# Optimization experiments

Measured on AMD Instinct MI355X. Metric: run time of the kernel, lower is better.

The kernel has to match this reference:

```python
import jax, jax.numpy as jnp
import numpy as np

L, B, H, S, V, D = 2, 128, 1024, 512, 32000, 64
W_SCALE = 0.02

def setup_inputs() -> dict:
    key = jax.random.key(0)
    ks = jax.random.split(key, 17)
    f = lambda k, shape: jax.random.normal(k, shape, dtype=jnp.float32)
    return {
        "input_ids": jax.random.randint(ks[0], (1, B), 0, V),
        "h": f(ks[1], (L, B, H)),
        "c": f(ks[2], (L, B, H)),
        "h_s": f(ks[3], (S, B, H)),
        "emb": f(ks[4], (V, H)),
        "W_pt": f(ks[5], (H, H)) * W_SCALE,
        "b_pt": f(ks[6], (H,)) * W_SCALE,
        "v_pt": f(ks[7], (H,)) * W_SCALE,
        "b_v": f(ks[8], (1,)) * W_SCALE,
        "W_a": f(ks[9], (H, H)) * W_SCALE,
        "b_a": f(ks[10], (1,)) * W_SCALE,
        "W_ih": f(ks[11], (L, 4 * H, H)) * W_SCALE,
        "W_hh": f(ks[12], (L, 4 * H, H)) * W_SCALE,
        "b_ih": f(ks[13], (L, 4 * H)) * W_SCALE,
        "b_hh": f(ks[14], (L, 4 * H)) * W_SCALE,
        "W_out": f(ks[15], (V, H)) * W_SCALE,
        "b_out": f(ks[16], (V,)) * W_SCALE,
    }


def reference(input_ids, h, c, h_s, emb, W_pt, b_pt, v_pt, b_v, W_a, b_a,
              W_ih, W_hh, b_ih, b_hh, W_out, b_out):
    S_len = h_s.shape[0]
    x_emb = emb[input_ids]                     # [1, B, H]
    h_top = h[-1]                              # [B, H] top-layer decoder state
    # predicted alignment position p_t = S * sigmoid(v . tanh(W h + b))
    p_t = S_len * jax.nn.sigmoid(jnp.tanh(h_top @ W_pt.T + b_pt) @ v_pt + b_v[0])  # [B]
    s = jnp.clip(jnp.round(p_t).astype(jnp.int32), D, S_len - 1 - D)               # [B]
    # gather local window h_s[s-D : s+D+1] per batch element
    idx = s[:, None] + jnp.arange(-D, D + 1)    # [B, 2D+1]
    h_s_b = jnp.transpose(h_s, (1, 0, 2))       # [B, S, H]
    h_loc = jnp.take_along_axis(h_s_b, idx[:, :, None], axis=1)  # [B, 2D+1, H]
    # bilinear score h_t^T W_a h_s_j per window position
    scores = jnp.einsum('bh,hk,bjk->bj', h_top, W_a, h_loc) + b_a[0]  # [B, 2D+1]
    sigma2 = (D / 2.0) ** 2
    gauss = jnp.exp(-((idx.astype(p_t.dtype) - p_t[:, None]) ** 2) / (2.0 * sigma2))
    a_t = jax.nn.softmax(scores, axis=-1) * gauss                      # [B, 2D+1]
    context = jnp.einsum('bj,bjh->bh', a_t, h_loc)                     # [B, H]
    # inject context into the LSTM hidden state, then run one step
    h_in = h + context[None]                    # [L, B, H]
    x = x_emb[0]                                # [B, H]
    hs, cs = [], []
    for l in range(h.shape[0]):
        gates = x @ W_ih[l].T + b_ih[l] + h_in[l] @ W_hh[l].T + b_hh[l]
        i, f, g, o = jnp.split(gates, 4, axis=-1)
        c_new = jax.nn.sigmoid(f) * c[l] + jax.nn.sigmoid(i) * jnp.tanh(g)
        h_new = jax.nn.sigmoid(o) * jnp.tanh(c_new)
        hs.append(h_new)
        cs.append(c_new)
        x = h_new
    h_out = jnp.stack(hs)                       # [L, B, H]
    c_out = jnp.stack(cs)                       # [L, B, H]
    logits = jax.nn.log_softmax(x @ W_out.T + b_out, axis=-1)  # [B, V]
    return logits, h_out, c_out, context, s
```

## Files before the change

### kernel.cpp

```cpp
#include <hip/hip_runtime.h>
#include <hip/hip_bf16.h>
#include <math.h>

typedef __bf16 bf16_8 __attribute__((ext_vector_type(8)));
typedef __bf16 bf16_4 __attribute__((ext_vector_type(4)));
typedef float  f32x4  __attribute__((ext_vector_type(4)));

static __device__ __forceinline__ float sigmoidf_(float x){ return 1.0f/(1.0f + expf(-x)); }

#define BB 128
#define HH 1024
#define SS 512
#define VV 32000

#define OFF_A0    0u
#define OFF_A1    524288u
#define OFF_ALOG  1048576u
#define OFF_AH    1310720u
#define OFF_AM    1572864u
#define OFF_AL    1835008u
#define OFF_WAT   2097152u
#define OFF_Q     6291456u
#define OFF_Z     6815744u
#define OFF_PT    7340032u
#define OFF_SI    7340544u
#define OFF_SC    7341056u
#define OFF_G0P   7408640u
#define OFF_G1P   24185856u
#define OFF_PMAX  40963072u
#define OFF_PSUM  41225216u

__global__ void k_prep_all(const float* __restrict__ W_a, float* __restrict__ WaT,
                           const int* __restrict__ ids, const float* __restrict__ emb,
                           const float* __restrict__ h, const float* __restrict__ b_pt,
                           __bf16* __restrict__ A0, __bf16* __restrict__ Ah,
                           __bf16* __restrict__ Am, __bf16* __restrict__ Al,
                           float* __restrict__ z, float* __restrict__ q){
  __shared__ float tsm[32][33];
  int blk = blockIdx.x, t = threadIdx.x;
  if (blk < 1024){
    int kt = blk & 31, nt = blk >> 5;
    int c = t & 31, r0 = t >> 5;
    #pragma unroll
    for (int i = 0; i < 4; ++i){
      int r = r0 + 8*i;
      tsm[r][c] = W_a[(size_t)(kt*32 + r)*HH + nt*32 + c];
    }
    __syncthreads();
    #pragma unroll
    for (int i = 0; i < 4; ++i){
      int r = r0 + 8*i;
      WaT[(size_t)(nt*32 + r)*HH + kt*32 + c] = tsm[c][r];
    }
  } else {
    int b = blk - 1024, c = t*4;
    int tok = ids[b];
    f32x4 e = *(const f32x4*)(emb + (size_t)tok*HH + c);
    bf16_4 e4;
    #pragma unroll
    for (int i=0;i<4;i++) e4[i] = (__bf16)e[i];
    *(bf16_4*)(A0 + (size_t)b*2048 + c) = e4;
    f32x4 x = *(const f32x4*)(h + (size_t)BB*HH + (size_t)b*HH + c);
    bf16_4 hi4, mi4, lo4;
    #pragma unroll
    for (int i=0;i<4;i++){
      float v = x[i];
      __bf16 bh = (__bf16)v; float r1 = v - (float)bh;
      __bf16 bm = (__bf16)r1; float r2 = r1 - (float)bm;
      hi4[i]=bh; mi4[i]=bm; lo4[i]=(__bf16)r2;
    }
    *(bf16_4*)(Ah + (size_t)b*HH + c) = hi4;
    *(bf16_4*)(Am + (size_t)b*HH + c) = mi4;
    *(bf16_4*)(Al + (size_t)b*HH + c) = lo4;
    *(f32x4*)(z + (size_t)b*HH + c) = *(const f32x4*)(b_pt + c);
    *(f32x4*)(q + (size_t)b*HH + c) = f32x4{0.f,0.f,0.f,0.f};
  }
}

template<int PREC>
__device__ __forceinline__ void gemm_small(
    char* smem,
    const __bf16* __restrict__ Ah, const __bf16* __restrict__ Am, const __bf16* __restrict__ Al,
    int lda, const float* __restrict__ B1, int K,
    float* __restrict__ C, int N, int xblk, int ysplit)
{
  constexpr int NS   = PREC;
  constexpr int BK   = 32;
  constexpr int KG   = BK/8;
  constexpr int TILE = 128*BK*2;
  constexpr int UPT  = (128*KG)/256;
  char* sA = smem;
  char* sB = smem + NS*TILE;

  const int t = threadIdx.x;
  const int lane = t & 63, wave = t >> 6;
  const int wm = wave >> 1, wn = wave & 1;
  const int quad = lane >> 4, ln = lane & 15;
  const int nblock = xblk * 128;
  const int kchunk = K / ysplit;
  const int kstart = blockIdx.y * kchunk;
  const int kend = kstart + kchunk;

  f32x4 acc[4][4];
  #pragma unroll
  for (int i=0;i<4;i++)
    #pragma unroll
    for (int j=0;j<4;j++) acc[i][j] = f32x4{0.f,0.f,0.f,0.f};

  for (int k0 = kstart; k0 < kend; k0 += BK){
    #pragma unroll
    for (int i = 0; i < UPT; ++i){
      int u = t + 256*i;
      int row = u / KG, kg = u % KG;
      int sl = row*(BK*2) + (((kg ^ (row & (KG-1)))) << 4);
      *(uint4*)(sA + sl) = *(const uint4*)(Ah + (size_t)row*lda + k0 + kg*8);
      if constexpr (PREC >= 2)
        *(uint4*)(sA + TILE + sl) = *(const uint4*)(Am + (size_t)row*lda + k0 + kg*8);
      if constexpr (PREC >= 3)
        *(uint4*)(sA + 2*TILE + sl) = *(const uint4*)(Al + (size_t)row*lda + k0 + kg*8);
      int ng = nblock + row;
      const float* src = B1 + (size_t)ng*K + k0 + kg*8;
      f32x4 x0 = *(const f32x4*)(src);
      f32x4 x1 = *(const f32x4*)(src + 4);
      bf16_8 hi, mi, lo;
      #pragma unroll
      for (int qv=0;qv<8;qv++){
        float v = (qv<4) ? x0[qv] : x1[qv-4];
        __bf16 bh = (__bf16)v;
        hi[qv] = bh;
        float r1 = v - (float)bh;
        __bf16 bm = (__bf16)r1;
        mi[qv] = bm;
        lo[qv] = (__bf16)(r1 - (float)bm);
      }
      *(bf16_8*)(sB + sl) = hi;
      if constexpr (PREC >= 2) *(bf16_8*)(sB + TILE + sl) = mi;
      if constexpr (PREC >= 3) *(bf16_8*)(sB + 2*TILE + sl) = lo;
    }
    __syncthreads();
    {
      bf16_8 af[NS][4], bfr[NS][4];
      #pragma unroll
      for (int mt=0; mt<4; ++mt){
        int row = wm*64 + mt*16 + ln;
        int kg = quad;
        int sl = row*(BK*2) + (((kg ^ (row & (KG-1)))) << 4);
        #pragma unroll
        for (int s=0;s<NS;s++) af[s][mt] = *(const bf16_8*)(sA + s*TILE + sl);
      }
      #pragma unroll
      for (int nt=0; nt<4; ++nt){
        int row = wn*64 + nt*16 + ln;
        int kg = quad;
        int sl = row*(BK*2) + (((kg ^ (row & (KG-1)))) << 4);
        #pragma unroll
        for (int s=0;s<NS;s++) bfr[s][nt] = *(const bf16_8*)(sB + s*TILE + sl);
      }
      #pragma unroll
      for (int mt=0; mt<4; ++mt)
        #pragma unroll
        for (int nt=0; nt<4; ++nt){
          acc[mt][nt] = __builtin_amdgcn_mfma_f32_16x16x32_bf16(af[0][mt], bfr[0][nt], acc[mt][nt], 0,0,0);
          if constexpr (PREC >= 2){
            acc[mt][nt] = __builtin_amdgcn_mfma_f32_16x16x32_bf16(af[0][mt], bfr[1][nt], acc[mt][nt], 0,0,0);
            acc[mt][nt] = __builtin_amdgcn_mfma_f32_16x16x32_bf16(af[1][mt], bfr[0][nt], acc[mt][nt], 0,0,0);
          }
          if constexpr (PREC >= 3){
            acc[mt][nt] = __builtin_amdgcn_mfma_f32_16x16x32_bf16(af[0][mt], bfr[2][nt], acc[mt][nt], 0,0,0);
            acc[mt][nt] = __builtin_amdgcn_mfma_f32_16x16x32_bf16(af[1][mt], bfr[1][nt], acc[mt][nt], 0,0,0);
            acc[mt][nt] = __builtin_amdgcn_mfma_f32_16x16x32_bf16(af[2][mt], bfr[0][nt], acc[mt][nt], 0,0,0);
          }
        }
    }
    __syncthreads();
  }

  #pragma unroll
  for (int nt=0; nt<4; ++nt){
    int n = nblock + wn*64 + nt*16 + ln;
    #pragma unroll
    for (int mt=0; mt<4; ++mt){
      int m0 = wm*64 + mt*16 + quad*4;
      #pragma unroll
      for (int r=0;r<4;++r)
        atomicAdd(C + (size_t)(m0 + r)*N + n, acc[mt][nt][r]);
    }
  }
}

__global__ __launch_bounds__(256) void k_qz(
    const __bf16* __restrict__ Ah, const __bf16* __restrict__ Am, const __bf16* __restrict__ Al,
    const float* __restrict__ WaT, const float* __restrict__ Wpt,
    float* __restrict__ q, float* __restrict__ z)
{
  __shared__ __align__(16) char smem[49152];
  if (blockIdx.x < 8)
    gemm_small<2>(smem, Ah, Am, nullptr, 1024, WaT, 1024, q, 1024, blockIdx.x, 8);
  else
    gemm_small<3>(smem, Ah, Am, Al, 1024, Wpt, 1024, z, 1024, blockIdx.x - 8, 8);
}

__global__ __launch_bounds__(256) void k_gates(
    const __bf16* __restrict__ Ain, int lda,
    const float* __restrict__ B1, const float* __restrict__ B2, int K1,
    float* __restrict__ C, int N)
{
  constexpr int BK  = 64;
  constexpr int KG  = BK/8;
  constexpr int TILE = 128*BK*2;
  constexpr int UPT = (128*KG)/256;
  __shared__ __align__(16) char smem[2*TILE];
  char* sA = smem;
  char* sB = smem + TILE;

  const int t = threadIdx.x;
  const int lane = t & 63, wave = t >> 6;
  const int wm = wave >> 1, wn = wave & 1;
  const int quad = lane >> 4, ln = lane & 15;
  const int nblock = blockIdx.x * 128;
  const int K = 2*K1;
  const int kchunk = K / gridDim.y;
  const int kstart = blockIdx.y * kchunk;
  const int kend = kstart + kchunk;

  f32x4 acc[4][4];
  #pragma unroll
  for (int i=0;i<4;i++)
    #pragma unroll
    for (int j=0;j<4;j++) acc[i][j] = f32x4{0.f,0.f,0.f,0.f};

  uint4 aR[UPT]; f32x4 bR[UPT][2];
  auto issue = [&](int k0){
    #pragma unroll
    for (int i=0;i<UPT;++i){
      int u = t + 256*i, row = u/KG, kg = u%KG;
      aR[i] = *(const uint4*)(Ain + (size_t)row*lda + k0 + kg*8);
      int ng = nblock + row;
      const float* src = (k0 < K1) ? (B1 + (size_t)ng*K1 + k0 + kg*8)
                                   : (B2 + (size_t)ng*K1 + (k0 - K1) + kg*8);
      bR[i][0] = *(const f32x4*)(src);
      bR[i][1] = *(const f32x4*)(src + 4);
    }
  };
  issue(kstart);
  for (int k0 = kstart; k0 < kend; k0 += BK){
    __syncthreads();
    #pragma unroll
    for (int i=0;i<UPT;++i){
      int u = t + 256*i, row = u/KG, kg = u%KG;
      int sl = row*(BK*2) + (((kg ^ (row & (KG-1)))) << 4);
      *(uint4*)(sA + sl) = aR[i];
      bf16_8 hi;
      #pragma unroll
      for (int qv=0;qv<8;++qv) hi[qv] = (__bf16)((qv<4) ? bR[i][0][qv] : bR[i][1][qv-4]);
      *(bf16_8*)(sB + sl) = hi;
    }
    __syncthreads();
    if (k0 + BK < kend) issue(k0 + BK);
    #pragma unroll
    for (int ks = 0; ks < BK/32; ++ks){
      bf16_8 af[4], bfr[4];
      #pragma unroll
      for (int mt=0; mt<4; ++mt){
        int row = wm*64 + mt*16 + ln;
        int kg = ks*4 + quad;
        int sl = row*(BK*2) + (((kg ^ (row & (KG-1)))) << 4);
        af[mt] = *(const bf16_8*)(sA + sl);
      }
      #pragma unroll
      for (int nt=0; nt<4; ++nt){
        int row = wn*64 + nt*16 + ln;
        int kg = ks*4 + quad;
        int sl = row*(BK*2) + (((kg ^ (row & (KG-1)))) << 4);
        bfr[nt] = *(const bf16_8*)(sB + sl);
      }
      #pragma unroll
      for (int mt=0; mt<4; ++mt)
        #pragma unroll
        for (int nt=0; nt<4; ++nt)
          acc[mt][nt] = __builtin_amdgcn_mfma_f32_16x16x32_bf16(af[mt], bfr[nt], acc[mt][nt], 0,0,0);
    }
  }

  float* Cp = C + (size_t)blockIdx.y * 128 * N;
  #pragma unroll
  for (int nt=0; nt<4; ++nt){
    int n = nblock + wn*64 + nt*16 + ln;
    #pragma unroll
    for (int mt=0; mt<4; ++mt){
      int m0 = wm*64 + mt*16 + quad*4;
      #pragma unroll
      for (int r=0;r<4;++r)
        Cp[(size_t)(m0 + r)*N + n] = acc[mt][nt][r];
    }
  }
}

__global__ __launch_bounds__(256) void k_logits(
    const __bf16* __restrict__ A, const float* __restrict__ Wout,
    const float* __restrict__ bias, float* __restrict__ C,
    float* __restrict__ Pmax, float* __restrict__ Psum)
{
  constexpr int BK = 64, KG = 8;
  constexpr int ATILE = 128*BK*2;
  constexpr int BTILE = 64*BK*2;
  __shared__ __align__(16) char smem[ATILE + BTILE];
  char* sA = smem;
  char* sB = smem + ATILE;

  const int t = threadIdx.x;
  const int lane = t & 63, wave = t >> 6;
  const int quad = lane >> 4, ln = lane & 15;
  const int nblock = blockIdx.x * 64;

  f32x4 acc[2][4];
  #pragma unroll
  for (int i=0;i<2;i++)
    #pragma unroll
    for (int j=0;j<4;j++) acc[i][j] = f32x4{0.f,0.f,0.f,0.f};

  uint4 aR[4]; f32x4 bR[2][2];
  auto issue = [&](int k0){
    #pragma unroll
    for (int i=0;i<4;++i){
      int u = t + 256*i, row = u >> 3, kg = u & 7;
      aR[i] = *(const uint4*)(A + (size_t)row*HH + k0 + kg*8);
    }
    #pragma unroll
    for (int i=0;i<2;++i){
      int u = t + 256*i, row = u >> 3, kg = u & 7;
      const float* src = Wout + (size_t)(nblock + row)*HH + k0 + kg*8;
      bR[i][0] = *(const f32x4*)(src);
      bR[i][1] = *(const f32x4*)(src + 4);
    }
  };
  issue(0);
  for (int k0 = 0; k0 < HH; k0 += BK){
    __syncthreads();
    #pragma unroll
    for (int i=0;i<4;++i){
      int u = t + 256*i, row = u >> 3, kg = u & 7;
      int sl = row*(BK*2) + ((kg ^ (row & 7)) << 4);
      *(uint4*)(sA + sl) = aR[i];
    }
    #pragma unroll
    for (int i=0;i<2;++i){
      int u = t + 256*i, row = u >> 3, kg = u & 7;
      int sl = row*(BK*2) + ((kg ^ (row & 7)) << 4);
      bf16_8 hi;
      #pragma unroll
      for (int qv=0;qv<8;++qv) hi[qv] = (__bf16)((qv<4) ? bR[i][0][qv] : bR[i][1][qv-4]);
      *(bf16_8*)(sB + sl) = hi;
    }
    __syncthreads();
    if (k0 + BK < HH) issue(k0 + BK);
    #pragma unroll
    for (int ks = 0; ks < BK/32; ++ks){
      bf16_8 af[2], bfr[4];
      #pragma unroll
      for (int mt=0; mt<2; ++mt){
        int row = wave*32 + mt*16 + ln;
        int kg = ks*4 + quad;
        int sl = row*(BK*2) + ((kg ^ (row & 7)) << 4);
        af[mt] = *(const bf16_8*)(sA + sl);
      }
      #pragma unroll
      for (int nt=0; nt<4; ++nt){
        int row = nt*16 + ln;
        int kg = ks*4 + quad;
        int sl = row*(BK*2) + ((kg ^ (row & 7)) << 4);
        bfr[nt] = *(const bf16_8*)(sB + sl);
      }
      #pragma unroll
      for (int mt=0; mt<2; ++mt)
        #pragma unroll
        for (int nt=0; nt<4; ++nt)
          acc[mt][nt] = __builtin_amdgcn_mfma_f32_16x16x32_bf16(af[mt], bfr[nt], acc[mt][nt], 0,0,0);
    }
  }

  #pragma unroll
  for (int mt=0; mt<2; ++mt)
    #pragma unroll
    for (int r=0; r<4; ++r){
      int row = wave*32 + mt*16 + quad*4 + r;
      float m4 = -1e30f;
      #pragma unroll
      for (int nt=0; nt<4; ++nt){
        int n = nblock + nt*16 + ln;
        m4 = fmaxf(m4, acc[mt][nt][r] + bias[n]);
      }
      #pragma unroll
      for (int m=1;m<16;m<<=1) m4 = fmaxf(m4, __shfl_xor(m4, m));
      float s4 = 0.f;
      #pragma unroll
      for (int nt=0; nt<4; ++nt){
        int n = nblock + nt*16 + ln;
        float v = acc[mt][nt][r] + bias[n];
        C[(size_t)row*VV + n] = v;
        s4 += expf(v - m4);
      }
      #pragma unroll
      for (int m=1;m<16;m<<=1) s4 += __shfl_xor(s4, m);
      if (ln == 0){
        Pmax[(size_t)blockIdx.x*128 + row] = m4;
        Psum[(size_t)blockIdx.x*128 + row] = s4;
      }
    }
}

__global__ __launch_bounds__(256) void k_scores(
    const float* __restrict__ z, const float* __restrict__ v_pt, const float* __restrict__ b_v,
    const float* __restrict__ q, const float* __restrict__ h_s,
    const float* __restrict__ b_a,
    float* __restrict__ sc, float* __restrict__ p_t, int* __restrict__ s_i,
    float* __restrict__ out_s)
{
  __shared__ float red[4];
  __shared__ float sh[2];
  int b = blockIdx.x, t = threadIdx.x;
  {
    f32x4 zv = *(const f32x4*)(z + (size_t)b*HH + t*4);
    f32x4 vv = *(const f32x4*)(v_pt + t*4);
    float ps = tanhf(zv[0])*vv[0] + tanhf(zv[1])*vv[1] + tanhf(zv[2])*vv[2] + tanhf(zv[3])*vv[3];
    #pragma unroll
    for (int m=1;m<64;m<<=1) ps += __shfl_xor(ps, m);
    if ((t&63)==0) red[t>>6] = ps;
    __syncthreads();
    if (t == 0){
      float tot = red[0]+red[1]+red[2]+red[3] + b_v[0];
      float p = (float)SS * sigmoidf_(tot);
      float sf = rintf(p);
      sf = fminf(fmaxf(sf, 64.0f), 447.0f);
      sh[0] = p; sh[1] = sf;
      if (blockIdx.y == 0){ p_t[b] = p; s_i[b] = (int)sf; out_s[b] = sf; }
    }
    __syncthreads();
  }
  int si = (int)sh[1];
  int jj = blockIdx.y*4 + (t >> 6);
  if (jj >= 129) return;
  int lane = t & 63;
  int pos = si - 64 + jj;
  const float* row = h_s + ((size_t)pos*BB + b)*HH;
  const float* qb  = q + (size_t)b*HH;
  f32x4 a = f32x4{0.f,0.f,0.f,0.f};
  #pragma unroll
  for (int c = lane*4; c < HH; c += 256){
    f32x4 r4 = *(const f32x4*)(row + c);
    f32x4 q4 = *(const f32x4*)(qb + c);
    a += r4*q4;
  }
  float sdot = a[0]+a[1]+a[2]+a[3];
  #pragma unroll
  for (int m=1;m<64;m<<=1) sdot += __shfl_xor(sdot, m);
  if (lane == 0) sc[b*132 + jj] = sdot + b_a[0];
}

__global__ __launch_bounds__(256) void k_context(
    const float* __restrict__ sc, const int* __restrict__ s_i, const float* __restrict__ p_t,
    const float* __restrict__ h_s, const float* __restrict__ h,
    float* __restrict__ ctx_out, __bf16* __restrict__ A0, __bf16* __restrict__ A1){
  __shared__ float sat[132];
  __shared__ float sctx[4][512];
  __shared__ int spos;
  int bb = blockIdx.x;
  int b = bb >> 1, half = bb & 1;
  int t = threadIdx.x, w = t >> 6, l = t & 63;
  if (w == 0){
    const float* scb = sc + b*132;
    float mx = -1e30f;
    for (int j=l; j<129; j+=64) mx = fmaxf(mx, scb[j]);
    #pragma unroll
    for (int m=1;m<64;m<<=1) mx = fmaxf(mx, __shfl_xor(mx, m));
    float sum = 0.f;
    for (int j=l; j<129; j+=64) sum += expf(scb[j] - mx);
    #pragma unroll
    for (int m=1;m<64;m<<=1) sum += __shfl_xor(sum, m);
    float inv = 1.0f/sum;
    float pt = p_t[b];
    int si = s_i[b];
    if (l == 0) spos = si - 64;
    float s0 = (float)(si - 64);
    for (int j=l; j<129; j+=64){
      float e = expf(scb[j]-mx)*inv;
      float d = (s0 + (float)j) - pt;
      sat[j] = e * expf(-(d*d) * (1.0f/2048.0f));
    }
  }
  __syncthreads();
  int pos0 = spos;
  int jstart = (w == 0) ? 0 : (33 + 32*(w-1));
  int jcnt   = (w == 0) ? 33 : 32;
  const float* base = h_s + ((size_t)pos0*BB + b)*HH + half*512;
  f32x4 acc0 = f32x4{0.f,0.f,0.f,0.f};
  f32x4 acc1 = f32x4{0.f,0.f,0.f,0.f};
  for (int j = jstart; j < jstart + jcnt; ++j){
    const float* row = base + (size_t)j*BB*HH;
    float aj = sat[j];
    acc0 += *(const f32x4*)(row + l*4) * aj;
    acc1 += *(const f32x4*)(row + 256 + l*4) * aj;
  }
  *(f32x4*)(&sctx[w][l*4])       = acc0;
  *(f32x4*)(&sctx[w][256 + l*4]) = acc1;
  __syncthreads();
  if (t < 128){
    int c = t*4;
    f32x4 v = *(f32x4*)(&sctx[0][c]) + *(f32x4*)(&sctx[1][c])
            + *(f32x4*)(&sctx[2][c]) + *(f32x4*)(&sctx[3][c]);
    int gc = half*512 + c;
    *(f32x4*)(ctx_out + (size_t)b*HH + gc) = v;
    f32x4 h0 = *(const f32x4*)(h + (size_t)b*HH + gc) + v;
    f32x4 h1 = *(const f32x4*)(h + (size_t)BB*HH + (size_t)b*HH + gc) + v;
    bf16_4 v0, v1;
    #pragma unroll
    for (int i=0;i<4;i++){ v0[i]=(__bf16)h0[i]; v1[i]=(__bf16)h1[i]; }
    *(bf16_4*)(A0 + (size_t)b*2048 + 1024 + gc) = v0;
    *(bf16_4*)(A1 + (size_t)b*2048 + 1024 + gc) = v1;
  }
}

__global__ void k_cell(const float* __restrict__ part,
                       const float* __restrict__ bih, const float* __restrict__ bhh,
                       const float* __restrict__ c_in,
                       float* __restrict__ h_out, float* __restrict__ c_out,
                       __bf16* __restrict__ Anext, int strideNext){
  int g = blockIdx.x*256 + threadIdx.x;
  int b = g >> 10, hc = g & 1023;
  float ig = bih[hc]        + bhh[hc];
  float fg = bih[1024 + hc] + bhh[1024 + hc];
  float gg = bih[2048 + hc] + bhh[2048 + hc];
  float og = bih[3072 + hc] + bhh[3072 + hc];
  #pragma unroll
  for (int y = 0; y < 8; ++y){
    const float* gb = part + ((size_t)y*BB + b)*4096;
    ig += gb[hc]; fg += gb[1024+hc]; gg += gb[2048+hc]; og += gb[3072+hc];
  }
  float cn = sigmoidf_(fg)*c_in[g] + sigmoidf_(ig)*tanhf(gg);
  float hn = sigmoidf_(og)*tanhf(cn);
  c_out[g] = cn; h_out[g] = hn;
  Anext[(size_t)b*strideNext + hc] = (__bf16)hn;
}

__global__ void k_lsesub(const float* __restrict__ Pmax, const float* __restrict__ Psum,
                         float* __restrict__ out){
  int b = blockIdx.y, l = threadIdx.x;
  float M = -1e30f;
  for (int i=l; i<500; i+=64) M = fmaxf(M, Pmax[(size_t)i*128 + b]);
  #pragma unroll
  for (int m=1;m<64;m<<=1) M = fmaxf(M, __shfl_xor(M, m));
  float s = 0.f;
  for (int i=l; i<500; i+=64) s += Psum[(size_t)i*128 + b] * expf(Pmax[(size_t)i*128 + b] - M);
  #pragma unroll
  for (int m=1;m<64;m<<=1) s += __shfl_xor(s, m);
  float L = M + logf(s);
  int i = blockIdx.x*256 + l*4;
  f32x4 v = *(f32x4*)(out + (size_t)b*VV + i);
  v[0]-=L; v[1]-=L; v[2]-=L; v[3]-=L;
  *(f32x4*)(out + (size_t)b*VV + i) = v;
}

extern "C" void kernel_launch(void* const* d_in, const int* in_sizes, int n_in,
                              void* d_out, int out_size, void* d_ws, size_t ws_size,
                              hipStream_t stream){
  const int*   ids   = (const int*)d_in[0];
  const float* h     = (const float*)d_in[1];
  const float* c     = (const float*)d_in[2];
  const float* h_s   = (const float*)d_in[3];
  const float* emb   = (const float*)d_in[4];
  const float* W_pt  = (const float*)d_in[5];
  const float* b_pt  = (const float*)d_in[6];
  const float* v_pt  = (const float*)d_in[7];
  const float* b_v   = (const float*)d_in[8];
  const float* W_a   = (const float*)d_in[9];
  const float* b_a   = (const float*)d_in[10];
  const float* W_ih  = (const float*)d_in[11];
  const float* W_hh  = (const float*)d_in[12];
  const float* b_ih  = (const float*)d_in[13];
  const float* b_hh  = (const float*)d_in[14];
  const float* W_out = (const float*)d_in[15];
  const float* b_out = (const float*)d_in[16];

  char* ws = (char*)d_ws;
  __bf16* A0   = (__bf16*)(ws + OFF_A0);
  __bf16* A1   = (__bf16*)(ws + OFF_A1);
  __bf16* Alog = (__bf16*)(ws + OFF_ALOG);
  __bf16* Ah   = (__bf16*)(ws + OFF_AH);
  __bf16* Am   = (__bf16*)(ws + OFF_AM);
  __bf16* Al   = (__bf16*)(ws + OFF_AL);
  float* WaT   = (float*)(ws + OFF_WAT);
  float* q     = (float*)(ws + OFF_Q);
  float* z     = (float*)(ws + OFF_Z);
  float* p_t   = (float*)(ws + OFF_PT);
  int*   s_i   = (int*)  (ws + OFF_SI);
  float* sc    = (float*)(ws + OFF_SC);
  float* g0p   = (float*)(ws + OFF_G0P);
  float* g1p   = (float*)(ws + OFF_G1P);
  float* Pmax  = (float*)(ws + OFF_PMAX);
  float* Psum  = (float*)(ws + OFF_PSUM);

  float* out        = (float*)d_out;
  float* out_logits = out;
  float* out_h      = out + 4096000;
  float* out_c      = out + 4358144;
  float* out_ctx    = out + 4620288;
  float* out_s      = out + 4751360;

  k_prep_all<<<1152, 256, 0, stream>>>(W_a, WaT, ids, emb, h, b_pt, A0, Ah, Am, Al, z, q);
  k_qz<<<dim3(16,8), 256, 0, stream>>>(Ah, Am, Al, WaT, W_pt, q, z);
  k_scores<<<dim3(128,33), 256, 0, stream>>>(z, v_pt, b_v, q, h_s, b_a, sc, p_t, s_i, out_s);
  k_context<<<256, 256, 0, stream>>>(sc, s_i, p_t, h_s, h, out_ctx, A0, A1);
  k_gates<<<dim3(32,8), 256, 0, stream>>>(A0, 2048, W_ih, W_hh, 1024, g0p, 4096);
  k_cell<<<512, 256, 0, stream>>>(g0p, b_ih, b_hh, c, out_h, out_c, A1, 2048);
  k_gates<<<dim3(32,8), 256, 0, stream>>>(A1, 2048, W_ih + 4194304, W_hh + 4194304, 1024, g1p, 4096);
  k_cell<<<512, 256, 0, stream>>>(g1p, b_ih + 4096, b_hh + 4096, c + 131072,
                                  out_h + 131072, out_c + 131072, Alog, 1024);
  k_logits<<<500, 256, 0, stream>>>(Alog, W_out, b_out, out_logits, Pmax, Psum);
  k_lsesub<<<dim3(125,128), 64, 0, stream>>>(Pmax, Psum, out_logits);
}
```

Before: 672.2 us.

## Halve split-K partitions in gates/qz and split context over window groups

The gate GEMMs and the q/z GEMMs now use 4 split-K partitions instead of 8. This halves the partial-sum buffers that k_cell must re-read and shrinks the workspace. The context kernel is reorganised so each block handles one batch row and one quarter of the window across all 1024 columns, writing partials. A new k_ctxfin kernel then reduces those partials and builds the bf16 LSTM inputs. The trade-off is fewer blocks for the GEMMs and one extra kernel launch plus a global partial round-trip for the context.

```diff
diff --git a/kernel.cpp b/kernel.cpp
--- a/kernel.cpp
+++ b/kernel.cpp
@@ -26,9 +26,10 @@
 #define OFF_SI    7340544u
 #define OFF_SC    7341056u
 #define OFF_G0P   7408640u
-#define OFF_G1P   24185856u
-#define OFF_PMAX  40963072u
-#define OFF_PSUM  41225216u
+#define OFF_G1P   15797248u
+#define OFF_PMAX  24185856u
+#define OFF_PSUM  24448000u
+#define OFF_PCTX  24710144u
 
 __global__ void k_prep_all(const float* __restrict__ W_a, float* __restrict__ WaT,
                            const int* __restrict__ ids, const float* __restrict__ emb,
@@ -195,9 +196,9 @@
 {
   __shared__ __align__(16) char smem[49152];
   if (blockIdx.x < 8)
-    gemm_small<2>(smem, Ah, Am, nullptr, 1024, WaT, 1024, q, 1024, blockIdx.x, 8);
+    gemm_small<2>(smem, Ah, Am, nullptr, 1024, WaT, 1024, q, 1024, blockIdx.x, 4);
   else
-    gemm_small<3>(smem, Ah, Am, Al, 1024, Wpt, 1024, z, 1024, blockIdx.x - 8, 8);
+    gemm_small<3>(smem, Ah, Am, Al, 1024, Wpt, 1024, z, 1024, blockIdx.x - 8, 4);
 }
 
 __global__ __launch_bounds__(256) void k_gates(
@@ -301,7 +302,7 @@
     const float* __restrict__ bias, float* __restrict__ C,
     float* __restrict__ Pmax, float* __restrict__ Psum)
 {
-  constexpr int BK = 64, KG = 8;
+  constexpr int BK = 64;
   constexpr int ATILE = 128*BK*2;
   constexpr int BTILE = 64*BK*2;
   __shared__ __align__(16) char smem[ATILE + BTILE];
@@ -459,13 +460,10 @@
 
 __global__ __launch_bounds__(256) void k_context(
     const float* __restrict__ sc, const int* __restrict__ s_i, const float* __restrict__ p_t,
-    const float* __restrict__ h_s, const float* __restrict__ h,
-    float* __restrict__ ctx_out, __bf16* __restrict__ A0, __bf16* __restrict__ A1){
+    const float* __restrict__ h_s, float* __restrict__ pctx){
   __shared__ float sat[132];
-  __shared__ float sctx[4][512];
   __shared__ int spos;
-  int bb = blockIdx.x;
-  int b = bb >> 1, half = bb & 1;
+  int b = blockIdx.x, jg = blockIdx.y;
   int t = threadIdx.x, w = t >> 6, l = t & 63;
   if (w == 0){
     const float* scb = sc + b*132;
@@ -490,34 +488,33 @@
   }
   __syncthreads();
   int pos0 = spos;
-  int jstart = (w == 0) ? 0 : (33 + 32*(w-1));
-  int jcnt   = (w == 0) ? 33 : 32;
-  const float* base = h_s + ((size_t)pos0*BB + b)*HH + half*512;
-  f32x4 acc0 = f32x4{0.f,0.f,0.f,0.f};
-  f32x4 acc1 = f32x4{0.f,0.f,0.f,0.f};
+  int jstart = (jg == 0) ? 0 : (33 + 32*(jg-1));
+  int jcnt   = (jg == 0) ? 33 : 32;
+  int col = w*256 + l*4;
+  const float* base = h_s + ((size_t)pos0*BB + b)*HH + col;
+  f32x4 acc = f32x4{0.f,0.f,0.f,0.f};
   for (int j = jstart; j < jstart + jcnt; ++j){
-    const float* row = base + (size_t)j*BB*HH;
-    float aj = sat[j];
-    acc0 += *(const f32x4*)(row + l*4) * aj;
-    acc1 += *(const f32x4*)(row + 256 + l*4) * aj;
-  }
-  *(f32x4*)(&sctx[w][l*4])       = acc0;
-  *(f32x4*)(&sctx[w][256 + l*4]) = acc1;
-  __syncthreads();
-  if (t < 128){
-    int c = t*4;
-    f32x4 v = *(f32x4*)(&sctx[0][c]) + *(f32x4*)(&sctx[1][c])
-            + *(f32x4*)(&sctx[2][c]) + *(f32x4*)(&sctx[3][c]);
-    int gc = half*512 + c;
-    *(f32x4*)(ctx_out + (size_t)b*HH + gc) = v;
-    f32x4 h0 = *(const f32x4*)(h + (size_t)b*HH + gc) + v;
-    f32x4 h1 = *(const f32x4*)(h + (size_t)BB*HH + (size_t)b*HH + gc) + v;
-    bf16_4 v0, v1;
-    #pragma unroll
-    for (int i=0;i<4;i++){ v0[i]=(__bf16)h0[i]; v1[i]=(__bf16)h1[i]; }
-    *(bf16_4*)(A0 + (size_t)b*2048 + 1024 + gc) = v0;
-    *(bf16_4*)(A1 + (size_t)b*2048 + 1024 + gc) = v1;
-  }
+    acc += *(const f32x4*)(base + (size_t)j*BB*HH) * sat[j];
+  }
+  *(f32x4*)(pctx + ((size_t)jg*BB + b)*HH + col) = acc;
+}
+
+__global__ void k_ctxfin(const float* __restrict__ pctx, const float* __restrict__ h,
+                         float* __restrict__ ctx_out, __bf16* __restrict__ A0,
+                         __bf16* __restrict__ A1){
+  int b = blockIdx.x, c = threadIdx.x*4;
+  f32x4 v = *(const f32x4*)(pctx + ((size_t)0*BB + b)*HH + c)
+          + *(const f32x4*)(pctx + ((size_t)1*BB + b)*HH + c)
+          + *(const f32x4*)(pctx + ((size_t)2*BB + b)*HH + c)
+          + *(const f32x4*)(pctx + ((size_t)3*BB + b)*HH + c);
+  *(f32x4*)(ctx_out + (size_t)b*HH + c) = v;
+  f32x4 h0 = *(const f32x4*)(h + (size_t)b*HH + c) + v;
+  f32x4 h1 = *(const f32x4*)(h + (size_t)BB*HH + (size_t)b*HH + c) + v;
+  bf16_4 v0, v1;
+  #pragma unroll
+  for (int i=0;i<4;i++){ v0[i]=(__bf16)h0[i]; v1[i]=(__bf16)h1[i]; }
+  *(bf16_4*)(A0 + (size_t)b*2048 + 1024 + c) = v0;
+  *(bf16_4*)(A1 + (size_t)b*2048 + 1024 + c) = v1;
 }
 
 __global__ void k_cell(const float* __restrict__ part,
@@ -532,7 +529,7 @@
   float gg = bih[2048 + hc] + bhh[2048 + hc];
   float og = bih[3072 + hc] + bhh[3072 + hc];
   #pragma unroll
-  for (int y = 0; y < 8; ++y){
+  for (int y = 0; y < 4; ++y){
     const float* gb = part + ((size_t)y*BB + b)*4096;
     ig += gb[hc]; fg += gb[1024+hc]; gg += gb[2048+hc]; og += gb[3072+hc];
   }
@@ -598,6 +595,7 @@
   float* g1p   = (float*)(ws + OFF_G1P);
   float* Pmax  = (float*)(ws + OFF_PMAX);
   float* Psum  = (float*)(ws + OFF_PSUM);
+  float* pctx  = (float*)(ws + OFF_PCTX);
 
   float* out        = (float*)d_out;
   float* out_logits = out;
@@ -607,12 +605,13 @@
   float* out_s      = out + 4751360;
 
   k_prep_all<<<1152, 256, 0, stream>>>(W_a, WaT, ids, emb, h, b_pt, A0, Ah, Am, Al, z, q);
-  k_qz<<<dim3(16,8), 256, 0, stream>>>(Ah, Am, Al, WaT, W_pt, q, z);
+  k_qz<<<dim3(16,4), 256, 0, stream>>>(Ah, Am, Al, WaT, W_pt, q, z);
   k_scores<<<dim3(128,33), 256, 0, stream>>>(z, v_pt, b_v, q, h_s, b_a, sc, p_t, s_i, out_s);
-  k_context<<<256, 256, 0, stream>>>(sc, s_i, p_t, h_s, h, out_ctx, A0, A1);
-  k_gates<<<dim3(32,8), 256, 0, stream>>>(A0, 2048, W_ih, W_hh, 1024, g0p, 4096);
+  k_context<<<dim3(128,4), 256, 0, stream>>>(sc, s_i, p_t, h_s, pctx);
+  k_ctxfin<<<128, 256, 0, stream>>>(pctx, h, out_ctx, A0, A1);
+  k_gates<<<dim3(32,4), 256, 0, stream>>>(A0, 2048, W_ih, W_hh, 1024, g0p, 4096);
   k_cell<<<512, 256, 0, stream>>>(g0p, b_ih, b_hh, c, out_h, out_c, A1, 2048);
-  k_gates<<<dim3(32,8), 256, 0, stream>>>(A1, 2048, W_ih + 4194304, W_hh + 4194304, 1024, g1p, 4096);
+  k_gates<<<dim3(32,4), 256, 0, stream>>>(A1, 2048, W_ih + 4194304, W_hh + 4194304, 1024, g1p, 4096);
   k_cell<<<512, 256, 0, stream>>>(g1p, b_ih + 4096, b_hh + 4096, c + 131072,
                                   out_h + 131072, out_c + 131072, Alog, 1024);
   k_logits<<<500, 256, 0, stream>>>(Alog, W_out, b_out, out_logits, Pmax, Psum);
```

Result: slower. 688.6 us (+2.4%).
